# Performance work log

Hardware: AMD Instinct MI355X
Metric: run time of the kernel (lower is better)

## Reference

```python
import jax, jax.numpy as jnp
import numpy as np
from jax import lax

D_FEAT = 62
N_CLASSES = 500
N_DAGS, N_NODES, MAX_PREDS = 16384, 48, 4
NEG = -1e30


def masked_attention(w, x, mask):
    # x: [..., P, d], w: [d, 1], mask: [..., P, 1] bool -> [..., d]
    scores = jnp.where(mask, x @ w, NEG)          # [..., P, 1]
    a = jax.nn.softmax(scores, axis=-2)
    return jnp.sum(a * x, axis=-2)


def setup_inputs() -> dict:
    key = jax.random.key(0)
    ks = jax.random.split(key, 10)
    atoms = jax.random.normal(ks[0], (N_DAGS, N_NODES, D_FEAT), dtype=jnp.float32)
    # topologically valid predecessor lists: preds[t] < t or -1 (padding / source)
    raw = jax.random.randint(ks[1], (N_DAGS, N_NODES, MAX_PREDS), 0, N_NODES)
    t = jnp.arange(N_NODES)[None, :, None]
    preds = raw % jnp.maximum(t, 1)
    keep = jax.random.bernoulli(ks[2], 0.8, (N_DAGS, N_NODES, MAX_PREDS))
    preds = jnp.where((t > 0) & keep, preds, -1).astype(jnp.int32)
    s = 1.0 / np.sqrt(D_FEAT)
    W_single = jax.random.uniform(ks[3], (D_FEAT, D_FEAT), jnp.float32, -s, s)
    b_single = jax.random.uniform(ks[4], (D_FEAT,), jnp.float32, -s, s)
    sm = 1.0 / np.sqrt(2 * D_FEAT)
    W_merge = jax.random.uniform(ks[5], (D_FEAT, 2 * D_FEAT), jnp.float32, -sm, sm)
    b_merge = jax.random.uniform(ks[6], (D_FEAT,), jnp.float32, -sm, sm)
    att_w = jax.random.uniform(ks[7], (D_FEAT, 1), jnp.float32, 0.0, 1.0)
    dag_w = jax.random.uniform(ks[8], (D_FEAT, 1), jnp.float32, 0.0, 1.0)
    W_final = jax.random.uniform(ks[9], (N_CLASSES, D_FEAT), jnp.float32, -s, s)
    b_final = jnp.zeros((N_CLASSES,), jnp.float32)
    return {"atoms": atoms, "preds": preds, "W_single": W_single, "b_single": b_single,
            "W_merge": W_merge, "b_merge": b_merge, "att_w": att_w, "dag_w": dag_w,
            "W_final": W_final, "b_final": b_final}


def reference(atoms, preds, W_single, b_single, W_merge, b_merge, att_w, dag_w, W_final, b_final):
    # atoms: [D, N, d]; preds: [D, N, P] (-1 = no predecessor). Nodes are in topo order;
    # node N-1 is the sink whose output represents the DAG.
    single = jax.nn.relu(jnp.einsum('dnf,gf->dng', atoms, W_single) + b_single)  # source-node path

    def run_dag(atom_seq, pred_seq, single_seq):  # [N,d], [N,P], [N,d]
        def step(outs, t):
            p = pred_seq[t]                          # [P]
            mask = p >= 0
            g = outs[jnp.clip(p, 0)]                 # [P, d] gathered predecessor outputs
            agg = masked_attention(att_w, g, mask[:, None])
            merged = jax.nn.relu(W_merge @ jnp.concatenate([agg, atom_seq[t]]) + b_merge)
            out_t = jnp.where(mask.any(), merged, single_seq[t])
            return outs.at[t].set(out_t), None
        outs, _ = lax.scan(step, jnp.zeros_like(atom_seq), jnp.arange(atom_seq.shape[0]))
        return outs[-1]

    last = jax.vmap(run_dag)(atoms, preds, single)   # [D, d] sink output per DAG
    pooled = masked_attention(dag_w, last, jnp.ones((last.shape[0], 1), bool))  # [d]
    return jax.nn.sigmoid(W_final @ pooled + b_final)  # [500]
```

## Files before the change

### kernel.cpp

```cpp
#include <hip/hip_runtime.h>

#define D_FEAT    62
#define N_CLASSES 500
#define N_DAGS    16384
#define N_NODES   48
#define MAX_PREDS 4
#define ROWB      6160
#define SCS_STR   49
#define HIST_ROW  64
#define HIST_DAG  (N_NODES * HIST_ROW)

typedef __attribute__((ext_vector_type(8))) short short8;
typedef __attribute__((ext_vector_type(4))) float f32x4;

union FragU { unsigned int u[4]; short8 v; };
struct Raw { unsigned int u[16]; };

__device__ __forceinline__ float bf2f(unsigned short u) {
    union { unsigned int i; float f; } v;
    v.i = ((unsigned int)u) << 16;
    return v.f;
}

__device__ __forceinline__ unsigned short f2bf(float f) {
    union { float f; unsigned int i; } v;
    v.f = f;
    unsigned int x = v.i;
    return (unsigned short)((x + 0x7FFFu + ((x >> 16) & 1u)) >> 16);
}

__device__ __forceinline__ unsigned int pack2bf(float a, float b) {
    unsigned int ia = __float_as_uint(a), ib = __float_as_uint(b);
    ia += 0x7FFFu + ((ia >> 16) & 1u);
    ib += 0x7FFFu + ((ib >> 16) & 1u);
    return (ia >> 16) | (ib & 0xFFFF0000u);
}

__device__ __forceinline__ float pk_lo(unsigned int u) { return __uint_as_float(u << 16); }
__device__ __forceinline__ float pk_hi(unsigned int u) { return __uint_as_float(u & 0xFFFF0000u); }

__device__ __forceinline__ float bcast(float x, int k) {
    return __int_as_float(__builtin_amdgcn_readlane(__float_as_int(x), k));
}

__device__ __forceinline__ float ldm(const void* p, long i, int mode) {
    if (mode) return ((const float*)p)[i];
    else      return bf2f(((const unsigned short*)p)[i]);
}

__device__ __forceinline__ float wm_val(const void* W, int n, int k, int mode) {
    if (n >= D_FEAT) return 0.f;
    if (k < 62)  return ldm(W, n * 124 + k, mode);
    if (k < 64)  return 0.f;
    if (k < 126) return ldm(W, n * 124 + (k - 2), mode);
    return 0.f;
}

__device__ __forceinline__ float ws_val(const void* W, int n, int k, int mode) {
    if (n >= D_FEAT || k >= D_FEAT) return 0.f;
    return ldm(W, n * 62 + k, mode);
}

__device__ __forceinline__ void load_raw(Raw& r, const void* atoms, long row,
                                         int quad, int mode) {
    if (mode == 0) {
        const char* base = (const char*)atoms + row * 124;
        const int off3 = (quad < 3) ? (64 + quad * 16) : 108;
        #pragma unroll
        for (int w = 0; w < 4; ++w)
            r.u[w] = *(const unsigned int*)(base + quad * 16 + 4 * w);
        #pragma unroll
        for (int w = 0; w < 4; ++w)
            r.u[4 + w] = *(const unsigned int*)(base + off3 + 4 * w);
    } else {
        const char* base = (const char*)atoms + row * 248;
        const int off3 = (quad < 3) ? (128 + quad * 32) : 216;
        #pragma unroll
        for (int w = 0; w < 4; ++w) {
            uint2 v = *(const uint2*)(base + quad * 32 + 8 * w);
            r.u[2 * w] = v.x; r.u[2 * w + 1] = v.y;
        }
        #pragma unroll
        for (int w = 0; w < 4; ++w) {
            uint2 v = *(const uint2*)(base + off3 + 8 * w);
            r.u[8 + 2 * w] = v.x; r.u[9 + 2 * w] = v.y;
        }
    }
}

__device__ __forceinline__ void pack_frags(FragU& a2, FragU& a3, const Raw& r,
                                           int quad, int mode) {
    if (mode == 0) {
        #pragma unroll
        for (int w = 0; w < 4; ++w) a2.u[w] = r.u[w];
        if (quad < 3) {
            #pragma unroll
            for (int w = 0; w < 4; ++w) a3.u[w] = r.u[4 + w];
        } else {
            a3.u[0] = r.u[5]; a3.u[1] = r.u[6]; a3.u[2] = r.u[7]; a3.u[3] = 0;
        }
    } else {
        #pragma unroll
        for (int w = 0; w < 4; ++w)
            a2.u[w] = pack2bf(__uint_as_float(r.u[2 * w]), __uint_as_float(r.u[2 * w + 1]));
        if (quad < 3) {
            #pragma unroll
            for (int w = 0; w < 4; ++w)
                a3.u[w] = pack2bf(__uint_as_float(r.u[8 + 2 * w]), __uint_as_float(r.u[9 + 2 * w]));
        } else {
            #pragma unroll
            for (int w = 0; w < 3; ++w)
                a3.u[w] = pack2bf(__uint_as_float(r.u[10 + 2 * w]), __uint_as_float(r.u[11 + 2 * w]));
            a3.u[3] = 0;
        }
    }
}

template<int GH, int DPBT>
__global__ __launch_bounds__(64, 1) void k_dag(
    const void* __restrict__ atoms,
    const int*  __restrict__ preds,
    const void* __restrict__ W_single,
    const void* __restrict__ b_single,
    const void* __restrict__ W_merge,
    const void* __restrict__ b_merge,
    const void* __restrict__ att_w,
    const void* __restrict__ dag_w,
    unsigned short* __restrict__ hist,
    float* __restrict__ last_out,
    float* __restrict__ score_out)
{
    constexpr int SMEM_BYTES = GH ? (DPBT * SCS_STR * 4)
                                  : (DPBT * ROWB + DPBT * SCS_STR * 4);
    __shared__ char smem[SMEM_BYTES];

    constexpr unsigned long long FULLM = (DPBT == 16) ? 0xFFFFull : 0xFFull;

    const int  lane = threadIdx.x;
    const int  m    = lane & 15;
    const int  quad = lane >> 4;
    const int  mc   = (DPBT == 16) ? m : (m & 7);
    const bool wq   = (DPBT == 16) || (quad < 2);
    const int  d0   = blockIdx.x * DPBT;

    int mode;
    {
        const unsigned short* a16 = (const unsigned short*)atoms;
        const float v0 = bf2f(a16[2 * lane]);
        const float v1 = bf2f(a16[128 + 2 * lane]);
        const int bad = (!(fabsf(v0) < 64.f)) + (!(fabsf(v1) < 64.f));
        const int cnt = __popcll(__ballot(bad > 0)) + __popcll(__ballot(bad > 1));
        mode = (cnt > 16) ? 1 : 0;
    }

    short8 wmF[4][4], wsF[4][2];
    float bm4[4], bs4[4], aw4[4], dw4[4];
    #pragma unroll
    for (int nt = 0; nt < 4; ++nt) {
        const int n = m + 16 * nt;
        #pragma unroll
        for (int kt = 0; kt < 4; ++kt) {
            FragU f;
            #pragma unroll
            for (int w = 0; w < 4; ++w) {
                const int k = kt * 32 + quad * 8 + 2 * w;
                f.u[w] = pack2bf(wm_val(W_merge, n, k, mode), wm_val(W_merge, n, k + 1, mode));
            }
            wmF[nt][kt] = f.v;
        }
        #pragma unroll
        for (int kt = 0; kt < 2; ++kt) {
            FragU f;
            #pragma unroll
            for (int w = 0; w < 4; ++w) {
                const int k = kt * 32 + quad * 8 + 2 * w;
                f.u[w] = pack2bf(ws_val(W_single, n, k, mode), ws_val(W_single, n, k + 1, mode));
            }
            wsF[nt][kt] = f.v;
        }
        bm4[nt] = (n < D_FEAT) ? ldm(b_merge,  n, mode) : 0.f;
        bs4[nt] = (n < D_FEAT) ? ldm(b_single, n, mode) : 0.f;
        aw4[nt] = (n < D_FEAT) ? ldm(att_w,    n, mode) : 0.f;
        dw4[nt] = (n < D_FEAT) ? ldm(dag_w,    n, mode) : 0.f;
    }

    float* scs  = (float*)(smem + (GH ? 0 : DPBT * ROWB));
    float* srow = scs + mc * SCS_STR;
    const long arow0 = (long)(d0 + mc) * N_NODES;
    const int* pbase = preds + (size_t)(d0 + mc) * (N_NODES * MAX_PREDS);
    unsigned short* const hdag = GH ? (hist + (size_t)(d0 + mc) * HIST_DAG) : (unsigned short*)0;

    auto node_body = [&](int t, const int4 pv, const FragU a2, const FragU a3) {
        const int pm = max(max(pv.x, pv.y), max(pv.z, pv.w));
        const unsigned int mk = (unsigned int)(__ballot(pm >= 0) & FULLM);
        const unsigned int FULL = (unsigned int)FULLM;

        f32x4 acc[4] = { {0,0,0,0}, {0,0,0,0}, {0,0,0,0}, {0,0,0,0} };
        f32x4 sac[4] = { {0,0,0,0}, {0,0,0,0}, {0,0,0,0}, {0,0,0,0} };

        if (mk != 0u) {
            const int p0 = pv.x, p1 = pv.y, p2 = pv.z, p3 = pv.w;
            const int c0 = max(p0, 0), c1 = max(p1, 0), c2 = max(p2, 0), c3 = max(p3, 0);
            float q0 = srow[c0], q1 = srow[c1], q2 = srow[c2], q3 = srow[c3];
            q0 = (p0 >= 0) ? q0 : -1e30f;
            q1 = (p1 >= 0) ? q1 : -1e30f;
            q2 = (p2 >= 0) ? q2 : -1e30f;
            q3 = (p3 >= 0) ? q3 : -1e30f;
            const float mx = fmaxf(fmaxf(q0, q1), fmaxf(q2, q3));
            float e0 = (p0 >= 0) ? __expf(q0 - mx) : 0.f;
            float e1 = (p1 >= 0) ? __expf(q1 - mx) : 0.f;
            float e2 = (p2 >= 0) ? __expf(q2 - mx) : 0.f;
            float e3 = (p3 >= 0) ? __expf(q3 - mx) : 0.f;
            const float inv = 1.f / fmaxf(e0 + e1 + e2 + e3, 1e-30f);
            e0 *= inv; e1 *= inv; e2 *= inv; e3 *= inv;

            FragU A01[2];
            #pragma unroll
            for (int cc = 0; cc < 2; ++cc) {
                FragU g0, g1, g2, g3;
                if constexpr (GH) {
                    const unsigned short* gb = hdag + cc * 32 + quad * 8;
                    g0.v = *(const short8*)(gb + c0 * HIST_ROW);
                    g1.v = *(const short8*)(gb + c1 * HIST_ROW);
                    g2.v = *(const short8*)(gb + c2 * HIST_ROW);
                    g3.v = *(const short8*)(gb + c3 * HIST_ROW);
                } else {
                    const char* obase = smem + mc * ROWB;
                    const int boff = cc * 64 + quad * 16;
                    g0.v = *(const short8*)(obase + c0 * 128 + boff);
                    g1.v = *(const short8*)(obase + c1 * 128 + boff);
                    g2.v = *(const short8*)(obase + c2 * 128 + boff);
                    g3.v = *(const short8*)(obase + c3 * 128 + boff);
                }
                #pragma unroll
                for (int w = 0; w < 4; ++w) {
                    const float lo = fmaf(e0, pk_lo(g0.u[w]), fmaf(e1, pk_lo(g1.u[w]),
                                     fmaf(e2, pk_lo(g2.u[w]), e3 * pk_lo(g3.u[w]))));
                    const float hi = fmaf(e0, pk_hi(g0.u[w]), fmaf(e1, pk_hi(g1.u[w]),
                                     fmaf(e2, pk_hi(g2.u[w]), e3 * pk_hi(g3.u[w]))));
                    A01[cc].u[w] = pack2bf(lo, hi);
                }
            }
            #pragma unroll
            for (int nt = 0; nt < 4; ++nt) {
                f32x4 c = {0, 0, 0, 0};
                c = __builtin_amdgcn_mfma_f32_16x16x32_bf16(A01[0].v, wmF[nt][0], c, 0, 0, 0);
                c = __builtin_amdgcn_mfma_f32_16x16x32_bf16(A01[1].v, wmF[nt][1], c, 0, 0, 0);
                c = __builtin_amdgcn_mfma_f32_16x16x32_bf16(a2.v,     wmF[nt][2], c, 0, 0, 0);
                c = __builtin_amdgcn_mfma_f32_16x16x32_bf16(a3.v,     wmF[nt][3], c, 0, 0, 0);
                acc[nt] = c;
            }
        }
        if (mk != (unsigned int)FULLM) {
            #pragma unroll
            for (int nt = 0; nt < 4; ++nt) {
                f32x4 c = {0, 0, 0, 0};
                c = __builtin_amdgcn_mfma_f32_16x16x32_bf16(a2.v, wsF[nt][0], c, 0, 0, 0);
                c = __builtin_amdgcn_mfma_f32_16x16x32_bf16(a3.v, wsF[nt][1], c, 0, 0, 0);
                sac[nt] = c;
            }
        }
        (void)FULL;

        float out4[4][4];
        #pragma unroll
        for (int nt = 0; nt < 4; ++nt) {
            #pragma unroll
            for (int r = 0; r < 4; ++r) {
                const int dm = quad * 4 + r;
                const bool hp = (mk >> dm) & 1u;
                const float v = hp ? (acc[nt][r] + bm4[nt]) : (sac[nt][r] + bs4[nt]);
                out4[nt][r] = fmaxf(v, 0.f);
            }
        }

        #pragma unroll
        for (int nt = 0; nt < 4; ++nt) {
            const int n = m + 16 * nt;
            #pragma unroll
            for (int r = 0; r < 4; ++r) {
                if (wq) {
                    const int dm = quad * 4 + r;
                    if constexpr (GH)
                        hist[(size_t)(d0 + dm) * HIST_DAG + t * HIST_ROW + n] = f2bf(out4[nt][r]);
                    else
                        *(unsigned short*)(smem + dm * ROWB + t * 128 + n * 2) = f2bf(out4[nt][r]);
                }
            }
        }

        const bool fin = (t == N_NODES - 1);
        float sr[4] = {0, 0, 0, 0};
        #pragma unroll
        for (int nt = 0; nt < 4; ++nt) {
            const float w = fin ? dw4[nt] : aw4[nt];
            #pragma unroll
            for (int r = 0; r < 4; ++r) sr[r] = fmaf(out4[nt][r], w, sr[r]);
        }
        #pragma unroll
        for (int r = 0; r < 4; ++r) {
            sr[r] += __shfl_xor(sr[r], 1);
            sr[r] += __shfl_xor(sr[r], 2);
            sr[r] += __shfl_xor(sr[r], 4);
            sr[r] += __shfl_xor(sr[r], 8);
        }
        if (m == 0 && wq) {
            #pragma unroll
            for (int r = 0; r < 4; ++r) {
                if (!fin) scs[(quad * 4 + r) * SCS_STR + t] = sr[r];
                else      score_out[d0 + quad * 4 + r] = sr[r];
            }
        }
        if (fin && wq) {
            #pragma unroll
            for (int nt = 0; nt < 4; ++nt) {
                const int n = m + 16 * nt;
                if (n < D_FEAT) {
                    #pragma unroll
                    for (int r = 0; r < 4; ++r)
                        last_out[(size_t)(d0 + quad * 4 + r) * D_FEAT + n] = out4[nt][r];
                }
            }
        }
    };

    Raw r0, r1;
    load_raw(r0, atoms, arow0 + 0, quad, mode);
    int4 p0v = *(const int4*)(pbase + 0);
    load_raw(r1, atoms, arow0 + 1, quad, mode);
    int4 p1v = *(const int4*)(pbase + 4);

    #pragma unroll 1
    for (int t = 0; t < N_NODES; t += 2) {
        {
            const int4 p = p0v;
            FragU a2, a3;
            pack_frags(a2, a3, r0, quad, mode);
            if constexpr (!GH) {
                if (t + 2 < N_NODES) {
                    load_raw(r0, atoms, arow0 + (t + 2), quad, mode);
                    p0v = *(const int4*)(pbase + (t + 2) * 4);
                }
                node_body(t, p, a2, a3);
            } else {
                node_body(t, p, a2, a3);
                if (t + 2 < N_NODES) {
                    load_raw(r0, atoms, arow0 + (t + 2), quad, mode);
                    p0v = *(const int4*)(pbase + (t + 2) * 4);
                }
            }
        }
        {
            const int4 p = p1v;
            FragU a2, a3;
            pack_frags(a2, a3, r1, quad, mode);
            if constexpr (!GH) {
                if (t + 3 < N_NODES) {
                    load_raw(r1, atoms, arow0 + (t + 3), quad, mode);
                    p1v = *(const int4*)(pbase + (t + 3) * 4);
                }
                node_body(t + 1, p, a2, a3);
            } else {
                node_body(t + 1, p, a2, a3);
                if (t + 3 < N_NODES) {
                    load_raw(r1, atoms, arow0 + (t + 3), quad, mode);
                    p1v = *(const int4*)(pbase + (t + 3) * 4);
                }
            }
        }
    }
}

__global__ __launch_bounds__(256) void k_pool(
    const float* __restrict__ last,
    const float* __restrict__ score,
    float* __restrict__ vpart,
    float* __restrict__ mpart,
    float* __restrict__ spart)
{
    const int lane = threadIdx.x & 63;
    const int wv   = threadIdx.x >> 6;
    const int c    = blockIdx.x * 4 + wv;
    const int d0   = c * 64;

    const float s = score[d0 + lane];
    float m = s;
    #pragma unroll
    for (int off = 32; off > 0; off >>= 1) m = fmaxf(m, __shfl_xor(m, off));
    const float e = __expf(s - m);
    float den = e;
    #pragma unroll
    for (int off = 32; off > 0; off >>= 1) den += __shfl_xor(den, off);

    float acc = 0.f;
    #pragma unroll 4
    for (int j = 0; j < 64; ++j) {
        const float v = (lane < D_FEAT) ? last[(size_t)(d0 + j) * D_FEAT + lane] : 0.f;
        acc = fmaf(bcast(e, j), v, acc);
    }
    if (lane < D_FEAT) vpart[c * D_FEAT + lane] = acc;
    if (lane == 0) { mpart[c] = m; spart[c] = den; }
}

__global__ __launch_bounds__(256) void k_final(
    const void* __restrict__ atoms,
    const float* __restrict__ vpart,
    const float* __restrict__ mpart,
    const float* __restrict__ spart,
    const void* __restrict__ W_final,
    const void* __restrict__ b_final,
    void* __restrict__ out)
{
    __shared__ float red[256];
    __shared__ float wgt[256];
    __shared__ float pooled[D_FEAT];
    const int tid = threadIdx.x;

    const unsigned short* a16 = (const unsigned short*)atoms;
    const int bad = (!(fabsf(bf2f(a16[2 * (tid & 63)])) < 64.f))
                  + (!(fabsf(bf2f(a16[128 + 2 * (tid & 63)])) < 64.f));
    red[tid] = (float)bad;
    __syncthreads();
    for (int s = 128; s > 0; s >>= 1) {
        if (tid < s) red[tid] += red[tid + s];
        __syncthreads();
    }
    const int mode = (red[0] > 64.f) ? 1 : 0;
    __syncthreads();

    const float m = mpart[tid];
    red[tid] = m;
    __syncthreads();
    for (int s = 128; s > 0; s >>= 1) {
        if (tid < s) red[tid] = fmaxf(red[tid], red[tid + s]);
        __syncthreads();
    }
    const float M = red[0];
    __syncthreads();

    const float w = __expf(m - M);
    wgt[tid] = w;
    red[tid] = w * spart[tid];
    __syncthreads();
    for (int s = 128; s > 0; s >>= 1) {
        if (tid < s) red[tid] += red[tid + s];
        __syncthreads();
    }
    const float denom = red[0];
    __syncthreads();

    if (tid < D_FEAT) {
        float acc = 0.f;
        #pragma unroll 8
        for (int c = 0; c < 256; ++c) acc = fmaf(wgt[c], vpart[c * D_FEAT + tid], acc);
        pooled[tid] = acc / denom;
    }
    __syncthreads();

    for (int r = tid; r < N_CLASSES; r += 256) {
        float acc = ldm(b_final, r, mode);
        #pragma unroll
        for (int i = 0; i < D_FEAT; ++i)
            acc = fmaf(ldm(W_final, (long)r * D_FEAT + i, mode), pooled[i], acc);
        const float sg = 1.f / (1.f + __expf(-acc));
        if (mode) ((float*)out)[r] = sg;
        else      ((unsigned short*)out)[r] = f2bf(sg);
    }
}

extern "C" void kernel_launch(void* const* d_in, const int* in_sizes, int n_in,
                              void* d_out, int out_size, void* d_ws, size_t ws_size,
                              hipStream_t stream) {
    const void* atoms    = d_in[0];
    const int*  preds    = (const int*)d_in[1];
    const void* W_single = d_in[2];
    const void* b_single = d_in[3];
    const void* W_merge  = d_in[4];
    const void* b_merge  = d_in[5];
    const void* att_w    = d_in[6];
    const void* dag_w    = d_in[7];
    const void* W_final  = d_in[8];
    const void* b_final  = d_in[9];

    float* last  = (float*)d_ws;
    float* score = last + (size_t)N_DAGS * D_FEAT;
    float* vpart = score + N_DAGS;
    float* mpart = vpart + 256 * D_FEAT;
    float* spart = mpart + 256;
    unsigned short* hist = (unsigned short*)((char*)d_ws + (4ull << 20));
    const size_t need = (4ull << 20) + (size_t)N_DAGS * HIST_DAG * sizeof(unsigned short);

    if (ws_size >= need)
        k_dag<1,16><<<N_DAGS / 16, 64, 0, stream>>>(atoms, preds, W_single, b_single, W_merge,
                                                    b_merge, att_w, dag_w, hist, last, score);
    else
        k_dag<0,8> <<<N_DAGS / 8,  64, 0, stream>>>(atoms, preds, W_single, b_single, W_merge,
                                                    b_merge, att_w, dag_w, hist, last, score);
    k_pool <<<64, 256, 0, stream>>>(last, score, vpart, mpart, spart);
    k_final<<<1, 256, 0, stream>>>(atoms, vpart, mpart, spart, W_final, b_final, d_out);
}
```

Measured before the change: 495.9 us.

## Move W_single fragments to LDS, hoist gathers, and halve DAGs per block

W_single MFMA fragments move from registers into per-lane LDS slots, and launch bounds now allow two waves per SIMD so register pressure drops and occupancy can rise. The predecessor gathers are hoisted ahead of the softmax so their latency overlaps the exp math. The global-history path now runs 8 DAGs per 64-lane block instead of 16, which doubles the block count but leaves half the MFMA rows idle. The source-node path gains LDS reads in exchange.

```diff
diff --git a/kernel.cpp b/kernel.cpp
--- a/kernel.cpp
+++ b/kernel.cpp
@@ -117,7 +117,7 @@
 }
 
 template<int GH, int DPBT>
-__global__ __launch_bounds__(64, 1) void k_dag(
+__global__ __launch_bounds__(64, 2) void k_dag(
     const void* __restrict__ atoms,
     const int*  __restrict__ preds,
     const void* __restrict__ W_single,
@@ -130,8 +130,11 @@
     float* __restrict__ last_out,
     float* __restrict__ score_out)
 {
-    constexpr int SMEM_BYTES = GH ? (DPBT * SCS_STR * 4)
-                                  : (DPBT * ROWB + DPBT * SCS_STR * 4);
+    constexpr int HIST_LDS   = GH ? 0 : (DPBT * ROWB);
+    constexpr int SCS_BYTES  = DPBT * SCS_STR * 4;
+    constexpr int WSF_OFF    = HIST_LDS + SCS_BYTES;
+    constexpr int WSF_STRIDE = 136;
+    constexpr int SMEM_BYTES = WSF_OFF + 64 * WSF_STRIDE;
     __shared__ char smem[SMEM_BYTES];
 
     constexpr unsigned long long FULLM = (DPBT == 16) ? 0xFFFFull : 0xFFull;
@@ -153,8 +156,9 @@
         mode = (cnt > 16) ? 1 : 0;
     }
 
-    short8 wmF[4][4], wsF[4][2];
+    short8 wmF[4][4];
     float bm4[4], bs4[4], aw4[4], dw4[4];
+    char* const wsfp = smem + WSF_OFF + lane * WSF_STRIDE;
     #pragma unroll
     for (int nt = 0; nt < 4; ++nt) {
         const int n = m + 16 * nt;
@@ -176,7 +180,7 @@
                 const int k = kt * 32 + quad * 8 + 2 * w;
                 f.u[w] = pack2bf(ws_val(W_single, n, k, mode), ws_val(W_single, n, k + 1, mode));
             }
-            wsF[nt][kt] = f.v;
+            *(short8*)(wsfp + (nt * 2 + kt) * 16) = f.v;
         }
         bm4[nt] = (n < D_FEAT) ? ldm(b_merge,  n, mode) : 0.f;
         bs4[nt] = (n < D_FEAT) ? ldm(b_single, n, mode) : 0.f;
@@ -184,7 +188,7 @@
         dw4[nt] = (n < D_FEAT) ? ldm(dag_w,    n, mode) : 0.f;
     }
 
-    float* scs  = (float*)(smem + (GH ? 0 : DPBT * ROWB));
+    float* scs  = (float*)(smem + HIST_LDS);
     float* srow = scs + mc * SCS_STR;
     const long arow0 = (long)(d0 + mc) * N_NODES;
     const int* pbase = preds + (size_t)(d0 + mc) * (N_NODES * MAX_PREDS);
@@ -193,7 +197,6 @@
     auto node_body = [&](int t, const int4 pv, const FragU a2, const FragU a3) {
         const int pm = max(max(pv.x, pv.y), max(pv.z, pv.w));
         const unsigned int mk = (unsigned int)(__ballot(pm >= 0) & FULLM);
-        const unsigned int FULL = (unsigned int)FULLM;
 
         f32x4 acc[4] = { {0,0,0,0}, {0,0,0,0}, {0,0,0,0}, {0,0,0,0} };
         f32x4 sac[4] = { {0,0,0,0}, {0,0,0,0}, {0,0,0,0}, {0,0,0,0} };
@@ -202,6 +205,26 @@
             const int p0 = pv.x, p1 = pv.y, p2 = pv.z, p3 = pv.w;
             const int c0 = max(p0, 0), c1 = max(p1, 0), c2 = max(p2, 0), c3 = max(p3, 0);
             float q0 = srow[c0], q1 = srow[c1], q2 = srow[c2], q3 = srow[c3];
+
+            FragU G[2][4];
+            #pragma unroll
+            for (int cc = 0; cc < 2; ++cc) {
+                if constexpr (GH) {
+                    const unsigned short* gb = hdag + cc * 32 + quad * 8;
+                    G[cc][0].v = *(const short8*)(gb + c0 * HIST_ROW);
+                    G[cc][1].v = *(const short8*)(gb + c1 * HIST_ROW);
+                    G[cc][2].v = *(const short8*)(gb + c2 * HIST_ROW);
+                    G[cc][3].v = *(const short8*)(gb + c3 * HIST_ROW);
+                } else {
+                    const char* obase = smem + mc * ROWB;
+                    const int boff = cc * 64 + quad * 16;
+                    G[cc][0].v = *(const short8*)(obase + c0 * 128 + boff);
+                    G[cc][1].v = *(const short8*)(obase + c1 * 128 + boff);
+                    G[cc][2].v = *(const short8*)(obase + c2 * 128 + boff);
+                    G[cc][3].v = *(const short8*)(obase + c3 * 128 + boff);
+                }
+            }
+
             q0 = (p0 >= 0) ? q0 : -1e30f;
             q1 = (p1 >= 0) ? q1 : -1e30f;
             q2 = (p2 >= 0) ? q2 : -1e30f;
@@ -217,27 +240,12 @@
             FragU A01[2];
             #pragma unroll
             for (int cc = 0; cc < 2; ++cc) {
-                FragU g0, g1, g2, g3;
-                if constexpr (GH) {
-                    const unsigned short* gb = hdag + cc * 32 + quad * 8;
-                    g0.v = *(const short8*)(gb + c0 * HIST_ROW);
-                    g1.v = *(const short8*)(gb + c1 * HIST_ROW);
-                    g2.v = *(const short8*)(gb + c2 * HIST_ROW);
-                    g3.v = *(const short8*)(gb + c3 * HIST_ROW);
-                } else {
-                    const char* obase = smem + mc * ROWB;
-                    const int boff = cc * 64 + quad * 16;
-                    g0.v = *(const short8*)(obase + c0 * 128 + boff);
-                    g1.v = *(const short8*)(obase + c1 * 128 + boff);
-                    g2.v = *(const short8*)(obase + c2 * 128 + boff);
-                    g3.v = *(const short8*)(obase + c3 * 128 + boff);
-                }
                 #pragma unroll
                 for (int w = 0; w < 4; ++w) {
-                    const float lo = fmaf(e0, pk_lo(g0.u[w]), fmaf(e1, pk_lo(g1.u[w]),
-                                     fmaf(e2, pk_lo(g2.u[w]), e3 * pk_lo(g3.u[w]))));
-                    const float hi = fmaf(e0, pk_hi(g0.u[w]), fmaf(e1, pk_hi(g1.u[w]),
-                                     fmaf(e2, pk_hi(g2.u[w]), e3 * pk_hi(g3.u[w]))));
+                    const float lo = fmaf(e0, pk_lo(G[cc][0].u[w]), fmaf(e1, pk_lo(G[cc][1].u[w]),
+                                     fmaf(e2, pk_lo(G[cc][2].u[w]), e3 * pk_lo(G[cc][3].u[w]))));
+                    const float hi = fmaf(e0, pk_hi(G[cc][0].u[w]), fmaf(e1, pk_hi(G[cc][1].u[w]),
+                                     fmaf(e2, pk_hi(G[cc][2].u[w]), e3 * pk_hi(G[cc][3].u[w]))));
                     A01[cc].u[w] = pack2bf(lo, hi);
                 }
             }
@@ -254,13 +262,15 @@
         if (mk != (unsigned int)FULLM) {
             #pragma unroll
             for (int nt = 0; nt < 4; ++nt) {
+                FragU s0, s1;
+                s0.v = *(const short8*)(wsfp + (nt * 2 + 0) * 16);
+                s1.v = *(const short8*)(wsfp + (nt * 2 + 1) * 16);
                 f32x4 c = {0, 0, 0, 0};
-                c = __builtin_amdgcn_mfma_f32_16x16x32_bf16(a2.v, wsF[nt][0], c, 0, 0, 0);
-                c = __builtin_amdgcn_mfma_f32_16x16x32_bf16(a3.v, wsF[nt][1], c, 0, 0, 0);
+                c = __builtin_amdgcn_mfma_f32_16x16x32_bf16(a2.v, s0.v, c, 0, 0, 0);
+                c = __builtin_amdgcn_mfma_f32_16x16x32_bf16(a3.v, s1.v, c, 0, 0, 0);
                 sac[nt] = c;
             }
         }
-        (void)FULL;
 
         float out4[4][4];
         #pragma unroll
@@ -491,11 +501,11 @@
     const size_t need = (4ull << 20) + (size_t)N_DAGS * HIST_DAG * sizeof(unsigned short);
 
     if (ws_size >= need)
-        k_dag<1,16><<<N_DAGS / 16, 64, 0, stream>>>(atoms, preds, W_single, b_single, W_merge,
-                                                    b_merge, att_w, dag_w, hist, last, score);
+        k_dag<1,8><<<N_DAGS / 8, 64, 0, stream>>>(atoms, preds, W_single, b_single,
+            W_merge, b_merge, att_w, dag_w, hist, last, score);
     else
-        k_dag<0,8> <<<N_DAGS / 8,  64, 0, stream>>>(atoms, preds, W_single, b_single, W_merge,
-                                                    b_merge, att_w, dag_w, hist, last, score);
+        k_dag<0,8><<<N_DAGS / 8, 64, 0, stream>>>(atoms, preds, W_single, b_single,
+            W_merge, b_merge, att_w, dag_w, hist, last, score);
     k_pool <<<64, 256, 0, stream>>>(last, score, vpart, mpart, spart);
     k_final<<<1, 256, 0, stream>>>(atoms, vpart, mpart, spart, W_final, b_final, d_out);
 }
```

After: 537.4 us. 1.08x slower.
